# Kernel optimization log

Measured on AMD Instinct MI355X. Metric: run time of the kernel, lower is better.

Reference implementation:

```python
import jax, jax.numpy as jnp
import numpy as np

MAXHD, MAXV, MINA, MAXA, DT = 100.0, 40.0, -6.0, 4.0, 0.1
UNITS, IN_DIM = 20, 12


def setup_inputs() -> dict:
    key = jax.random.key(0)
    ks = jax.random.split(key, 12)
    nveh, nt = 8192, 1000
    lead_fol_inputs = jax.random.uniform(ks[0], (nveh, nt, 12), dtype=jnp.float32) * 50.0
    init_state = jax.random.uniform(ks[1], (nveh, 2), dtype=jnp.float32) * 20.0
    h0 = jnp.zeros((nveh, UNITS), jnp.float32)
    c0 = jnp.zeros((nveh, UNITS), jnp.float32)
    s = 0.1
    return {
        'lead_fol_inputs': lead_fol_inputs,
        'init_state': init_state,
        'h0': h0,
        'c0': c0,
        'lstm_kernel': jax.random.normal(ks[2], (IN_DIM, 4 * UNITS), jnp.float32) * s,
        'lstm_rec_kernel': jax.random.normal(ks[3], (UNITS, 4 * UNITS), jnp.float32) * s,
        'lstm_bias': jnp.zeros((4 * UNITS,), jnp.float32),
        'd2_w': jax.random.normal(ks[4], (UNITS, 10), jnp.float32) * s,
        'd2_b': jnp.zeros((10,), jnp.float32),
        'lc_w': jax.random.normal(ks[5], (10, 3), jnp.float32) * s,
        'lc_b': jnp.zeros((3,), jnp.float32),
        'd1_w': jax.random.normal(ks[6], (10, 1), jnp.float32) * s,
        'd1_b': jnp.zeros((1,), jnp.float32),
    }


def reference(lead_fol_inputs, init_state, h0, c0, lstm_kernel, lstm_rec_kernel,
              lstm_bias, d2_w, d2_b, lc_w, lc_b, d1_w, d1_b):
    # lead_fol_inputs: (nveh, nt, 12) -> scan over time axis
    xs = jnp.transpose(lead_fol_inputs, (1, 0, 2))  # (nt, nveh, 12)
    pos0 = init_state[:, 0]
    spd0 = init_state[:, 1]

    def step(carry, inp):
        pos, spd, h, c = carry
        lead_hd = (inp[:, :3] - pos[:, None]) / MAXHD
        fol_hd = (pos[:, None] - inp[:, 3:6]) / MAXHD
        spds = inp[:, 6:] / MAXV
        cur = jnp.concatenate([lead_hd, fol_hd, spds], axis=1)  # (nveh, 12)
        cur = jnp.where(jnp.isnan(cur), jnp.ones_like(cur), cur)
        # Keras LSTMCell: gate order i, f, g, o
        z = cur @ lstm_kernel + h @ lstm_rec_kernel + lstm_bias
        i, f, g, o = jnp.split(z, 4, axis=1)
        c = jax.nn.sigmoid(f) * c + jax.nn.sigmoid(i) * jnp.tanh(g)
        h = jax.nn.sigmoid(o) * jnp.tanh(c)
        x = jax.nn.relu(h @ d2_w + d2_b)          # dense2, (nveh, 10)
        lc = x @ lc_w + lc_b                      # lc_actions, (nveh, 3)
        acc_raw = (x @ d1_w + d1_b)[:, 0]         # dense1, (nveh,)
        acc = (MAXA - MINA) * acc_raw + MINA
        pos = pos + DT * spd
        spd = spd + DT * acc
        return (pos, spd, h, c), (pos, lc)

    (pos_f, spd_f, h_f, c_f), (pos_seq, lc_seq) = jax.lax.scan(
        step, (pos0, spd0, h0, c0), xs)
    pos_outputs = jnp.transpose(pos_seq, (1, 0))        # (nveh, nt)
    lc_outputs = jnp.transpose(lc_seq, (1, 0, 2))       # (nveh, nt, 3)
    curspeed = spd_f[:, None]                            # (nveh, 1)
    return pos_outputs, lc_outputs, curspeed, (h_f, c_f)
```

## Files before the change

### kernel.cpp

```cpp
#include <hip/hip_runtime.h>
#include <hip/hip_bf16.h>


typedef __attribute__((ext_vector_type(8))) short short8;
typedef __attribute__((ext_vector_type(4))) short short4v;
typedef __attribute__((ext_vector_type(4))) float float4v;
typedef __attribute__((ext_vector_type(2))) float float2v;

__device__ __forceinline__ short f2b(float f) {
    unsigned u = __float_as_uint(f);
    u += 0x7fffu + ((u >> 16) & 1u);
    return (short)(u >> 16);
}

__device__ __forceinline__ float fast_exp2(float x) {
#if __has_builtin(__builtin_amdgcn_exp2f)
    return __builtin_amdgcn_exp2f(x);
#else
    return exp2f(x);
#endif
}
__device__ __forceinline__ float fast_rcp(float x) {
#if __has_builtin(__builtin_amdgcn_rcpf)
    return __builtin_amdgcn_rcpf(x);
#else
    return 1.0f / x;
#endif
}

#define L2E 1.44269504088896340736f

__global__ void __launch_bounds__(128) rnncf_kernel(
    const float* __restrict__ inp,
    const float* __restrict__ init_state,
    const float* __restrict__ h0g,
    const float* __restrict__ c0g,
    const float* __restrict__ Wk,
    const float* __restrict__ Wr,
    const float* __restrict__ bz_g,
    const float* __restrict__ W2,
    const float* __restrict__ b2_g,
    const float* __restrict__ Wlc,
    const float* __restrict__ blc,
    const float* __restrict__ Wd1,
    const float* __restrict__ bd1,
    float* __restrict__ out)
{
    __shared__ short h_lds[2][16 * 36];
    __shared__ float x_lds[2][16 * 12];
    __shared__ float pos_lds[2][16];

    const int tid = threadIdx.x;
    const int wv  = tid >> 6;
    const int l   = tid & 63;
    const int q   = l >> 4;
    const int col = l & 15;
    const int v0  = (blockIdx.x * 2 + wv) * 16;

    short* hl = h_lds[wv];
    float* xl = x_lds[wv];
    float* pl = pos_lds[wv];

    float* out_pos = out;
    float* out_lc  = out + 8192000;
    float* out_spd = out + 32768000;
    float* out_h   = out + 32776192;
    float* out_c   = out + 32940032;

    const float sgt[4] = {-L2E, -L2E, 2.0f * L2E, -L2E};
    const int g  = col & 3;
    const int cu = col >> 2;
    short8  w1t[5];
    float4v bz1[5];
#pragma unroll
    for (int p = 0; p < 5; ++p) {
        const int n = g * 20 + 4 * p + cu;
#pragma unroll
        for (int j = 0; j < 8; ++j) {
            int k = 8 * q + j;
            float wvl = (k < 12) ? Wk[k * 80 + n] : Wr[(k - 12) * 80 + n];
            w1t[p][j] = f2b(wvl * sgt[g]);
        }
#pragma unroll
        for (int r = 0; r < 4; ++r)
            bz1[p][r] = sgt[r] * bz_g[r * 20 + 4 * p + q];
    }
    short8 w2t;
#pragma unroll
    for (int j = 0; j < 8; ++j) {
        int k = 8 * q + j;
        float v = (col < 10 && k < 20) ? W2[k * 10 + col] : 0.0f;
        w2t[j] = f2b(v);
    }
    float4v bx;
#pragma unroll
    for (int r = 0; r < 4; ++r) { int n = 4 * q + r; bx[r] = (n < 10) ? b2_g[n] : 0.0f; }

    const int dm = l >> 2, dj = l & 3;
    float wd[10], bd;
#pragma unroll
    for (int n = 0; n < 10; ++n) wd[n] = (dj < 3) ? Wlc[n * 3 + dj] : Wd1[n];
    bd = (dj < 3) ? blc[dj] : bd1[0];

    float c_st[5], h_keep[5];
#pragma unroll
    for (int p = 0; p < 5; ++p) {
        c_st[p] = c0g[(size_t)(v0 + col) * 20 + 4 * p + q];
        h_keep[p] = 0.0f;
    }
    for (int i = l; i < 16 * 36; i += 64) hl[i] = 0;
#pragma unroll
    for (int p = 0; p < 5; ++p)
        hl[col * 36 + 4 * p + q] = f2b(h0g[(size_t)(v0 + col) * 20 + 4 * p + q]);

    float pos = 0.0f, spd = 0.0f;
    if (dj == 3) {
        pos = init_state[(size_t)(v0 + dm) * 2 + 0];
        spd = init_state[(size_t)(v0 + dm) * 2 + 1];
        pl[dm] = pos;
    }

    const float* ipbase = inp + (size_t)(v0 + col) * 12000;
    float4v inA = {0, 0, 0, 0}, inB = {0, 0, 0, 0}, inC = {0, 0, 0, 0};
    if (q == 0)      { inA = *(const float4v*)(ipbase + 0); inB = *(const float4v*)(ipbase + 4); }
    else if (q == 1) { inC = *(const float4v*)(ipbase + 8); }

    for (int t = 0; t < 1000; ++t) {
        float posv = pl[col];

        if (dj == 3) {
            pos += 0.1f * spd;
            pl[dm] = pos;
            out_pos[(size_t)(v0 + dm) * 1000 + t] = pos;
        }

        short8 bfrag;
        if (q == 0) {
            float pp = posv * 0.01f;
            bfrag[0] = f2b(__builtin_fmaf(inA[0],  0.01f, -pp));
            bfrag[1] = f2b(__builtin_fmaf(inA[1],  0.01f, -pp));
            bfrag[2] = f2b(__builtin_fmaf(inA[2],  0.01f, -pp));
            bfrag[3] = f2b(__builtin_fmaf(inA[3], -0.01f,  pp));
            bfrag[4] = f2b(__builtin_fmaf(inB[0], -0.01f,  pp));
            bfrag[5] = f2b(__builtin_fmaf(inB[1], -0.01f,  pp));
            bfrag[6] = f2b(inB[2] * 0.025f);
            bfrag[7] = f2b(inB[3] * 0.025f);
        } else if (q == 1) {
            bfrag[0] = f2b(inC[0] * 0.025f);
            bfrag[1] = f2b(inC[1] * 0.025f);
            bfrag[2] = f2b(inC[2] * 0.025f);
            bfrag[3] = f2b(inC[3] * 0.025f);
            short4v hv = *(const short4v*)&hl[col * 36 + 0];
            bfrag[4] = hv[0]; bfrag[5] = hv[1]; bfrag[6] = hv[2]; bfrag[7] = hv[3];
        } else {
            int off = (q == 2) ? 4 : 12;
            short4v ha = *(const short4v*)&hl[col * 36 + off];
            short4v hb = *(const short4v*)&hl[col * 36 + off + 4];
            bfrag[0] = ha[0]; bfrag[1] = ha[1]; bfrag[2] = ha[2]; bfrag[3] = ha[3];
            bfrag[4] = hb[0]; bfrag[5] = hb[1]; bfrag[6] = hb[2]; bfrag[7] = hb[3];
        }

        {
            int tn = (t < 999) ? t + 1 : 999;
            const float* ipn = ipbase + tn * 12;
            if (q == 0)      { inA = *(const float4v*)ipn; inB = *(const float4v*)(ipn + 4); }
            else if (q == 1) { inC = *(const float4v*)(ipn + 8); }
        }

        float4v z[5];
#pragma unroll
        for (int p = 0; p < 5; ++p)
            z[p] = __builtin_amdgcn_mfma_f32_16x16x32_bf16(w1t[p], bfrag, bz1[p], 0, 0, 0);

#pragma unroll
        for (int p = 0; p < 5; ++p) {
            float zi = fminf(fmaxf(z[p][0], -29.f), 29.f);
            float zf = fminf(fmaxf(z[p][1], -29.f), 29.f);
            float zg = fminf(fmaxf(z[p][2], -58.f), 58.f);
            float zo = fminf(fmaxf(z[p][3], -29.f), 29.f);
            float eA = fast_exp2(zi);
            float eB = fast_exp2(zf);
            float eC = fast_exp2(zg);
            float eD = fast_exp2(zo);
            float pA = 1.0f + eA, pB = 1.0f + eB, pC = eC + 1.0f, mC = eC - 1.0f;
            float t1 = pA * pC;
            float R  = fast_rcp(t1 * pB);
            float cn = (c_st[p] * t1 + mC * pB) * R;
            c_st[p] = cn;
            float ec = fminf(fmaxf(cn * (2.0f * L2E), -58.f), 58.f);
            float eE = fast_exp2(ec);
            float h  = (eE - 1.0f) * fast_rcp((1.0f + eD) * (eE + 1.0f));
            h_keep[p] = h;
            hl[col * 36 + 4 * p + q] = f2b(h);
        }

        short8 hfrag;
        {
            short4v ha = *(const short4v*)&hl[col * 36 + 8 * q];
            short4v hb = *(const short4v*)&hl[col * 36 + 8 * q + 4];
            hfrag[0] = ha[0]; hfrag[1] = ha[1]; hfrag[2] = ha[2]; hfrag[3] = ha[3];
            hfrag[4] = hb[0]; hfrag[5] = hb[1]; hfrag[6] = hb[2]; hfrag[7] = hb[3];
        }
        float4v x4 = __builtin_amdgcn_mfma_f32_16x16x32_bf16(w2t, hfrag, bx, 0, 0, 0);
        if (q < 3) {
            float4v xr;
#pragma unroll
            for (int r = 0; r < 4; ++r) xr[r] = fmaxf(x4[r], 0.0f);
            *(float4v*)&xl[col * 12 + 4 * q] = xr;
        }

        {
            float4v xa = *(const float4v*)&xl[dm * 12 + 0];
            float4v xb = *(const float4v*)&xl[dm * 12 + 4];
            float2v xc = *(const float2v*)&xl[dm * 12 + 8];
            float dot = bd;
            dot = __builtin_fmaf(xa[0], wd[0], dot);
            dot = __builtin_fmaf(xa[1], wd[1], dot);
            dot = __builtin_fmaf(xa[2], wd[2], dot);
            dot = __builtin_fmaf(xa[3], wd[3], dot);
            dot = __builtin_fmaf(xb[0], wd[4], dot);
            dot = __builtin_fmaf(xb[1], wd[5], dot);
            dot = __builtin_fmaf(xb[2], wd[6], dot);
            dot = __builtin_fmaf(xb[3], wd[7], dot);
            dot = __builtin_fmaf(xc[0], wd[8], dot);
            dot = __builtin_fmaf(xc[1], wd[9], dot);
            if (dj < 3) {
                out_lc[(size_t)(v0 + dm) * 3000 + t * 3 + dj] = dot;
            } else {
                float acc = 10.0f * dot - 6.0f;
                spd += 0.1f * acc;
            }
        }
    }

    if (dj == 3) out_spd[v0 + dm] = spd;
#pragma unroll
    for (int p = 0; p < 5; ++p) {
        out_h[(size_t)(v0 + col) * 20 + 4 * p + q] = h_keep[p];
        out_c[(size_t)(v0 + col) * 20 + 4 * p + q] = c_st[p];
    }
}

extern "C" void kernel_launch(void* const* d_in, const int* in_sizes, int n_in,
                              void* d_out, int out_size, void* d_ws, size_t ws_size,
                              hipStream_t stream) {
    rnncf_kernel<<<256, 128, 0, stream>>>(
        (const float*)d_in[0],  (const float*)d_in[1],  (const float*)d_in[2],
        (const float*)d_in[3],  (const float*)d_in[4],  (const float*)d_in[5],
        (const float*)d_in[6],  (const float*)d_in[7],  (const float*)d_in[8],
        (const float*)d_in[9],  (const float*)d_in[10], (const float*)d_in[11],
        (const float*)d_in[12], (float*)d_out);
}
```

Baseline: 1.511 ms.

## Replace LDS dense-head exchange with cross-lane shuffles and vectorize h LDS writes

Removes the x_lds and pos_lds shared buffers. Every lane now keeps pos/spd for its own vehicle column, and the dense-head dot products are reduced with __shfl_xor across quads instead of through a round trip in LDS. Hidden units are remapped so each lane writes four contiguous bf16 h values with one vector store. The next step's h fragments are preloaded right after that store, and the input prefetch is moved after the MFMAs. It also drops the lower clamps on the gate exponent inputs and unrolls the time loop by two, all to shorten the serial per-step dependency chain at the cost of redundant per-lane scalar work.

```diff
diff --git a/kernel.cpp b/kernel.cpp
--- a/kernel.cpp
+++ b/kernel.cpp
@@ -1,5 +1,4 @@
 #include <hip/hip_runtime.h>
-#include <hip/hip_bf16.h>
 
 
 typedef __attribute__((ext_vector_type(8))) short short8;
@@ -47,8 +46,6 @@
     float* __restrict__ out)
 {
     __shared__ short h_lds[2][16 * 36];
-    __shared__ float x_lds[2][16 * 12];
-    __shared__ float pos_lds[2][16];
 
     const int tid = threadIdx.x;
     const int wv  = tid >> 6;
@@ -57,9 +54,8 @@
     const int col = l & 15;
     const int v0  = (blockIdx.x * 2 + wv) * 16;
 
-    short* hl = h_lds[wv];
-    float* xl = x_lds[wv];
-    float* pl = pos_lds[wv];
+    short* hl  = h_lds[wv];
+    char*  hl8 = (char*)hl;
 
     float* out_pos = out;
     float* out_lc  = out + 8192000;
@@ -67,24 +63,30 @@
     float* out_h   = out + 32776192;
     float* out_c   = out + 32940032;
 
-    const float sgt[4] = {-L2E, -L2E, 2.0f * L2E, -L2E};
     const int g  = col & 3;
     const int cu = col >> 2;
+    const float sg_a = (g == 2) ? 2.0f * L2E : -L2E;
+
     short8  w1t[5];
     float4v bz1[5];
 #pragma unroll
     for (int p = 0; p < 5; ++p) {
-        const int n = g * 20 + 4 * p + cu;
+        const int ua = (p < 4) ? (4 * cu + p) : (16 + cu);
+        const int n  = g * 20 + ua;
 #pragma unroll
         for (int j = 0; j < 8; ++j) {
             int k = 8 * q + j;
             float wvl = (k < 12) ? Wk[k * 80 + n] : Wr[(k - 12) * 80 + n];
-            w1t[p][j] = f2b(wvl * sgt[g]);
-        }
-#pragma unroll
-        for (int r = 0; r < 4; ++r)
-            bz1[p][r] = sgt[r] * bz_g[r * 20 + 4 * p + q];
-    }
+            w1t[p][j] = f2b(wvl * sg_a);
+        }
+        const int ud = (p < 4) ? (4 * q + p) : (16 + q);
+#pragma unroll
+        for (int r = 0; r < 4; ++r) {
+            float sr = (r == 2) ? 2.0f * L2E : -L2E;
+            bz1[p][r] = sr * bz_g[r * 20 + ud];
+        }
+    }
+
     short8 w2t;
 #pragma unroll
     for (int j = 0; j < 8; ++j) {
@@ -96,47 +98,58 @@
 #pragma unroll
     for (int r = 0; r < 4; ++r) { int n = 4 * q + r; bx[r] = (n < 10) ? b2_g[n] : 0.0f; }
 
-    const int dm = l >> 2, dj = l & 3;
-    float wd[10], bd;
-#pragma unroll
-    for (int n = 0; n < 10; ++n) wd[n] = (dj < 3) ? Wlc[n * 3 + dj] : Wd1[n];
-    bd = (dj < 3) ? blc[dj] : bd1[0];
+    float wd3[4][4];
+#pragma unroll
+    for (int r = 0; r < 4; ++r) {
+        int f = 4 * q + r;
+#pragma unroll
+        for (int o = 0; o < 4; ++o)
+            wd3[r][o] = (f < 10) ? ((o < 3) ? Wlc[f * 3 + o] : Wd1[f]) : 0.0f;
+    }
+    const float lc_bias = (q < 3) ? blc[q] : 0.0f;
+    const float bd1v    = bd1[0];
+
+    const int base = col * 72;
+    const int o1 = (q == 0) ? 0 : (q == 1) ? 16 : (q == 2) ? 32 : 24;
+    const int o2 = (q == 0) ? 8 : (q == 1) ? 24 : (q == 2) ? 8  : 32;
+    const int o3 = (q == 2) ? 16 : 0;
+    const int a1 = base + o1, a2 = base + o2, a3 = base + o3;
+    const int awr = base + 8 * q;
 
     float c_st[5], h_keep[5];
 #pragma unroll
     for (int p = 0; p < 5; ++p) {
-        c_st[p] = c0g[(size_t)(v0 + col) * 20 + 4 * p + q];
+        const int ud = (p < 4) ? (4 * q + p) : (16 + q);
+        c_st[p] = c0g[(size_t)(v0 + col) * 20 + ud];
         h_keep[p] = 0.0f;
     }
     for (int i = l; i < 16 * 36; i += 64) hl[i] = 0;
-#pragma unroll
-    for (int p = 0; p < 5; ++p)
-        hl[col * 36 + 4 * p + q] = f2b(h0g[(size_t)(v0 + col) * 20 + 4 * p + q]);
-
-    float pos = 0.0f, spd = 0.0f;
-    if (dj == 3) {
-        pos = init_state[(size_t)(v0 + dm) * 2 + 0];
-        spd = init_state[(size_t)(v0 + dm) * 2 + 1];
-        pl[dm] = pos;
-    }
+    {
+        short4v h0w;
+#pragma unroll
+        for (int p = 0; p < 4; ++p)
+            h0w[p] = f2b(h0g[(size_t)(v0 + col) * 20 + 4 * q + p]);
+        *(short4v*)(hl8 + awr) = h0w;
+        hl[col * 36 + 16 + q] = f2b(h0g[(size_t)(v0 + col) * 20 + 16 + q]);
+    }
+
+    float2v ps = *(const float2v*)(init_state + (size_t)(v0 + col) * 2);
+    float pos = ps[0], spd = ps[1];
 
     const float* ipbase = inp + (size_t)(v0 + col) * 12000;
     float4v inA = {0, 0, 0, 0}, inB = {0, 0, 0, 0}, inC = {0, 0, 0, 0};
-    if (q == 0)      { inA = *(const float4v*)(ipbase + 0); inB = *(const float4v*)(ipbase + 4); }
+    if (q == 0)      { inA = *(const float4v*)(ipbase); inB = *(const float4v*)(ipbase + 4); }
     else if (q == 1) { inC = *(const float4v*)(ipbase + 8); }
 
+    short4v r1 = *(const short4v*)(hl8 + a1);
+    short4v r2 = *(const short4v*)(hl8 + a2);
+    short4v r3 = *(const short4v*)(hl8 + a3);
+
+#pragma unroll 2
     for (int t = 0; t < 1000; ++t) {
-        float posv = pl[col];
-
-        if (dj == 3) {
-            pos += 0.1f * spd;
-            pl[dm] = pos;
-            out_pos[(size_t)(v0 + dm) * 1000 + t] = pos;
-        }
-
         short8 bfrag;
         if (q == 0) {
-            float pp = posv * 0.01f;
+            float pp = pos * 0.01f;
             bfrag[0] = f2b(__builtin_fmaf(inA[0],  0.01f, -pp));
             bfrag[1] = f2b(__builtin_fmaf(inA[1],  0.01f, -pp));
             bfrag[2] = f2b(__builtin_fmaf(inA[2],  0.01f, -pp));
@@ -150,34 +163,35 @@
             bfrag[1] = f2b(inC[1] * 0.025f);
             bfrag[2] = f2b(inC[2] * 0.025f);
             bfrag[3] = f2b(inC[3] * 0.025f);
-            short4v hv = *(const short4v*)&hl[col * 36 + 0];
-            bfrag[4] = hv[0]; bfrag[5] = hv[1]; bfrag[6] = hv[2]; bfrag[7] = hv[3];
+            bfrag[4] = r3[0]; bfrag[5] = r3[1]; bfrag[6] = r3[2]; bfrag[7] = r3[3];
+        } else if (q == 2) {
+            bfrag[0] = r2[0]; bfrag[1] = r2[1]; bfrag[2] = r2[2]; bfrag[3] = r2[3];
+            bfrag[4] = r3[0]; bfrag[5] = r3[1]; bfrag[6] = r3[2]; bfrag[7] = r3[3];
         } else {
-            int off = (q == 2) ? 4 : 12;
-            short4v ha = *(const short4v*)&hl[col * 36 + off];
-            short4v hb = *(const short4v*)&hl[col * 36 + off + 4];
-            bfrag[0] = ha[0]; bfrag[1] = ha[1]; bfrag[2] = ha[2]; bfrag[3] = ha[3];
-            bfrag[4] = hb[0]; bfrag[5] = hb[1]; bfrag[6] = hb[2]; bfrag[7] = hb[3];
-        }
+            bfrag[0] = r1[0]; bfrag[1] = r1[1]; bfrag[2] = r1[2]; bfrag[3] = r1[3];
+            bfrag[4] = r2[0]; bfrag[5] = r2[1]; bfrag[6] = r2[2]; bfrag[7] = r2[3];
+        }
+
+        float4v z[5];
+#pragma unroll
+        for (int p = 0; p < 5; ++p)
+            z[p] = __builtin_amdgcn_mfma_f32_16x16x32_bf16(w1t[p], bfrag, bz1[p], 0, 0, 0);
 
         {
             int tn = (t < 999) ? t + 1 : 999;
             const float* ipn = ipbase + tn * 12;
-            if (q == 0)      { inA = *(const float4v*)ipn; inB = *(const float4v*)(ipn + 4); }
+            if (q == 0)      { inA = *(const float4v*)(ipn); inB = *(const float4v*)(ipn + 4); }
             else if (q == 1) { inC = *(const float4v*)(ipn + 8); }
         }
 
-        float4v z[5];
-#pragma unroll
-        for (int p = 0; p < 5; ++p)
-            z[p] = __builtin_amdgcn_mfma_f32_16x16x32_bf16(w1t[p], bfrag, bz1[p], 0, 0, 0);
-
+        short4v hw;
+        short h16 = 0;
 #pragma unroll
         for (int p = 0; p < 5; ++p) {
-            float zi = fminf(fmaxf(z[p][0], -29.f), 29.f);
-            float zf = fminf(fmaxf(z[p][1], -29.f), 29.f);
-            float zg = fminf(fmaxf(z[p][2], -58.f), 58.f);
-            float zo = fminf(fmaxf(z[p][3], -29.f), 29.f);
+            float zi = fminf(z[p][0], 29.f);
+            float zf = fminf(z[p][1], 29.f);
+            float zg = fminf(z[p][2], 58.f);
+            float zo = fminf(z[p][3], 29.f);
             float eA = fast_exp2(zi);
             float eB = fast_exp2(zf);
             float eC = fast_exp2(zg);
@@ -187,57 +201,57 @@
             float R  = fast_rcp(t1 * pB);
             float cn = (c_st[p] * t1 + mC * pB) * R;
             c_st[p] = cn;
-            float ec = fminf(fmaxf(cn * (2.0f * L2E), -58.f), 58.f);
+            float ec = fminf(cn * (2.0f * L2E), 58.f);
             float eE = fast_exp2(ec);
             float h  = (eE - 1.0f) * fast_rcp((1.0f + eD) * (eE + 1.0f));
             h_keep[p] = h;
-            hl[col * 36 + 4 * p + q] = f2b(h);
-        }
+            short hb = f2b(h);
+            if (p < 4) hw[p] = hb; else h16 = hb;
+        }
+        *(short4v*)(hl8 + awr) = hw;
+        hl[col * 36 + 16 + q] = h16;
+
+        r1 = *(const short4v*)(hl8 + a1);
+        r2 = *(const short4v*)(hl8 + a2);
+        r3 = *(const short4v*)(hl8 + a3);
 
         short8 hfrag;
-        {
-            short4v ha = *(const short4v*)&hl[col * 36 + 8 * q];
-            short4v hb = *(const short4v*)&hl[col * 36 + 8 * q + 4];
-            hfrag[0] = ha[0]; hfrag[1] = ha[1]; hfrag[2] = ha[2]; hfrag[3] = ha[3];
-            hfrag[4] = hb[0]; hfrag[5] = hb[1]; hfrag[6] = hb[2]; hfrag[7] = hb[3];
-        }
+        hfrag[0] = r1[0]; hfrag[1] = r1[1]; hfrag[2] = r1[2]; hfrag[3] = r1[3];
+        hfrag[4] = r2[0]; hfrag[5] = r2[1]; hfrag[6] = r2[2]; hfrag[7] = r2[3];
         float4v x4 = __builtin_amdgcn_mfma_f32_16x16x32_bf16(w2t, hfrag, bx, 0, 0, 0);
-        if (q < 3) {
-            float4v xr;
-#pragma unroll
-            for (int r = 0; r < 4; ++r) xr[r] = fmaxf(x4[r], 0.0f);
-            *(float4v*)&xl[col * 12 + 4 * q] = xr;
-        }
-
-        {
-            float4v xa = *(const float4v*)&xl[dm * 12 + 0];
-            float4v xb = *(const float4v*)&xl[dm * 12 + 4];
-            float2v xc = *(const float2v*)&xl[dm * 12 + 8];
-            float dot = bd;
-            dot = __builtin_fmaf(xa[0], wd[0], dot);
-            dot = __builtin_fmaf(xa[1], wd[1], dot);
-            dot = __builtin_fmaf(xa[2], wd[2], dot);
-            dot = __builtin_fmaf(xa[3], wd[3], dot);
-            dot = __builtin_fmaf(xb[0], wd[4], dot);
-            dot = __builtin_fmaf(xb[1], wd[5], dot);
-            dot = __builtin_fmaf(xb[2], wd[6], dot);
-            dot = __builtin_fmaf(xb[3], wd[7], dot);
-            dot = __builtin_fmaf(xc[0], wd[8], dot);
-            dot = __builtin_fmaf(xc[1], wd[9], dot);
-            if (dj < 3) {
-                out_lc[(size_t)(v0 + dm) * 3000 + t * 3 + dj] = dot;
-            } else {
-                float acc = 10.0f * dot - 6.0f;
-                spd += 0.1f * acc;
-            }
-        }
-    }
-
-    if (dj == 3) out_spd[v0 + dm] = spd;
+        float xr[4];
+#pragma unroll
+        for (int r = 0; r < 4; ++r) xr[r] = fmaxf(x4[r], 0.0f);
+
+        float pd[4];
+#pragma unroll
+        for (int o = 0; o < 4; ++o) {
+            float s = xr[0] * wd3[0][o];
+            s = __builtin_fmaf(xr[1], wd3[1][o], s);
+            s = __builtin_fmaf(xr[2], wd3[2][o], s);
+            s = __builtin_fmaf(xr[3], wd3[3][o], s);
+            s += __shfl_xor(s, 16);
+            s += __shfl_xor(s, 32);
+            pd[o] = s;
+        }
+        float lcv = pd[0];
+        lcv = (q == 1) ? pd[1] : lcv;
+        lcv = (q == 2) ? pd[2] : lcv;
+        if (q < 3)
+            out_lc[(size_t)(v0 + col) * 3000 + t * 3 + q] = lcv + lc_bias;
+
+        pos = __builtin_fmaf(0.1f, spd, pos);
+        if (q == 0) out_pos[(size_t)(v0 + col) * 1000 + t] = pos;
+        float acc = __builtin_fmaf(10.0f, pd[3] + bd1v, -6.0f);
+        spd = __builtin_fmaf(0.1f, acc, spd);
+    }
+
+    if (q == 0) out_spd[v0 + col] = spd;
 #pragma unroll
     for (int p = 0; p < 5; ++p) {
-        out_h[(size_t)(v0 + col) * 20 + 4 * p + q] = h_keep[p];
-        out_c[(size_t)(v0 + col) * 20 + 4 * p + q] = c_st[p];
+        const int ud = (p < 4) ? (4 * q + p) : (16 + q);
+        out_h[(size_t)(v0 + col) * 20 + ud] = h_keep[p];
+        out_c[(size_t)(v0 + col) * 20 + ud] = c_st[p];
     }
 }
 
```

Result: faster. 1.338 ms (-11.4%).
